# Kernel tuning notes

Measured on AMD Instinct MI355X. Metric: run time of the kernel, lower is better.

The kernel has to match this reference:

```python
import jax, jax.numpy as jnp
import numpy as np

FEATS = 32
N = FEATS + 1                      # graph nodes (node 0 = hub, 1..FEATS = leaves)
HID = FEATS * FEATS                # GRU hidden size
IN_GRU = (FEATS + 1) * FEATS * (2 * FEATS + 1)  # 33*32*65 = 68640
NEG_SLOPE = 0.2                    # DGL GATConv default leaky_relu slope


def _gat(x, W, al, ar, b):
    """DGL GATConv on the star graph (edges u->0 for all u incl. self-loop,
    plus self-loops on every node). x: [N,1]; W: [1, H*out]; al/ar: [H,out]; b: [H*out].
    Nodes 1..N-1 only receive their self-loop (softmax over one edge -> alpha=1),
    node 0 aggregates over all N source nodes."""
    H, out = al.shape
    z = (x @ W).reshape(-1, H, out)                       # [N,H,out]
    el = jnp.einsum('nho,ho->nh', z, al)                  # [N,H]
    er = jnp.einsum('nho,ho->nh', z, ar)                  # [N,H]
    e0 = jax.nn.leaky_relu(el + er[0], NEG_SLOPE)         # edges into node 0
    alpha = jax.nn.softmax(e0, axis=0)                    # softmax over N sources
    agg0 = jnp.einsum('nh,nho->ho', alpha, z)             # node-0 output
    return z.at[0].set(agg0) + b.reshape(1, H, out)


def _gru_cell(x, h, w_ih, w_hh, b_ih, b_hh):
    gi = w_ih @ x + b_ih
    gh = w_hh @ h + b_hh
    i_r, i_z, i_n = jnp.split(gi, 3)
    h_r, h_z, h_n = jnp.split(gh, 3)
    r = jax.nn.sigmoid(i_r + h_r)
    zg = jax.nn.sigmoid(i_z + h_z)
    n = jnp.tanh(i_n + r * h_n)
    return (1.0 - zg) * n + zg * h


def setup_inputs() -> dict:
    key = jax.random.key(0)
    ks = jax.random.split(key, 18)
    s = 0.05
    f32 = jnp.float32
    return {
        'data':   jax.random.normal(ks[0], (FEATS * FEATS,), f32),
        'hidden': jax.random.normal(ks[1], (2, 1, HID), f32),
        # feature GAT: in=1, out=FEATS, heads=FEATS
        'Wf':  jax.random.normal(ks[2], (1, FEATS * FEATS), f32) * s,
        'alf': jax.random.normal(ks[3], (FEATS, FEATS), f32) * s,
        'arf': jax.random.normal(ks[4], (FEATS, FEATS), f32) * s,
        'bf':  jax.random.normal(ks[5], (FEATS * FEATS,), f32) * s,
        # time GAT: in=1, out=FEATS, heads=1
        'Wt':  jax.random.normal(ks[6], (1, FEATS), f32) * s,
        'alt': jax.random.normal(ks[7], (1, FEATS), f32) * s,
        'art': jax.random.normal(ks[8], (1, FEATS), f32) * s,
        'bt':  jax.random.normal(ks[9], (FEATS,), f32) * s,
        # GRU: input IN_GRU, hidden HID, 2 layers
        'w_ih0': jax.random.normal(ks[10], (3 * HID, IN_GRU), f32) * s,
        'w_hh0': jax.random.normal(ks[11], (3 * HID, HID), f32) * s,
        'b_ih0': jax.random.normal(ks[12], (3 * HID,), f32) * s,
        'b_hh0': jax.random.normal(ks[13], (3 * HID,), f32) * s,
        'w_ih1': jax.random.normal(ks[14], (3 * HID, HID), f32) * s,
        'w_hh1': jax.random.normal(ks[15], (3 * HID, HID), f32) * s,
        'b_ih1': jax.random.normal(ks[16], (3 * HID,), f32) * s,
        'b_hh1': jax.random.normal(ks[17], (3 * HID,), f32) * s,
    }


def reference(data, hidden, Wf, alf, arf, bf, Wt, alt, art, bt,
              w_ih0, w_hh0, b_ih0, b_hh0, w_ih1, w_hh1, b_ih1, b_hh1):
    d = data.reshape(FEATS, FEATS)                         # [n_window, n_feats]
    # feature GAT on last window step, prepended with a zero for hub node 0
    data_r = jnp.concatenate([jnp.zeros((1,), d.dtype), d[-1]]).reshape(-1, 1)
    feat_r = _gat(data_r, Wf, alf, arf, bf)                # [N, FEATS, FEATS]
    # time GAT: one call per feature-row (data[:][i] == data[i]); vmapped
    Xt = jnp.concatenate([jnp.zeros((FEATS, 1), d.dtype), d], axis=1)[..., None]  # [FEATS, N, 1]
    tout = jax.vmap(lambda x: _gat(x, Wt, alt, art, bt))(Xt)  # [FEATS, N, 1, FEATS]
    time_r = tout[:, :, 0, :].transpose(1, 0, 2)           # concat on head dim -> [N, FEATS, FEATS]
    d3 = jnp.concatenate([jnp.zeros((1, FEATS), d.dtype), d]).reshape(N, FEATS, 1)
    x_in = jnp.concatenate([d3, feat_r, time_r], axis=2).reshape(-1)  # [IN_GRU]
    # 2-layer GRU, seq_len=1, batch=1
    h0 = _gru_cell(x_in, hidden[0, 0], w_ih0, w_hh0, b_ih0, b_hh0)
    h1 = _gru_cell(h0, hidden[1, 0], w_ih1, w_hh1, b_ih1, b_hh1)
    return h1, jnp.stack([h0, h1]).reshape(2, 1, HID)
```

## Files before the change

kernel.cpp:

```cpp
#include <hip/hip_runtime.h>
#include <math.h>

#define FEATS 32
#define NNODE 33
#define HID   1024
#define INGRU 68640
#define ROWS3 3072
#define N4BIG 17160
#define CHUNKS 8
#define CHLEN  2145
#define CHMAIN 2048
#define CHTAIL 97

typedef float f4 __attribute__((ext_vector_type(4)));

__device__ __forceinline__ float lrelu(float x) { return x > 0.f ? x : 0.2f * x; }
__device__ __forceinline__ float sigm(float x)  { return 1.f / (1.f + expf(-x)); }
__device__ __forceinline__ float dot4(f4 a, f4 b) {
    return a.x * b.x + a.y * b.y + a.z * b.z + a.w * b.w;
}

__global__ void __launch_bounds__(256) prep_kernel(
    const float* __restrict__ data,
    const float* __restrict__ Wf, const float* __restrict__ alf,
    const float* __restrict__ bf,
    const float* __restrict__ Wt, const float* __restrict__ alt,
    const float* __restrict__ bt,
    float* __restrict__ x_in, float* __restrict__ gi0_zero)
{
    const int n = blockIdx.x;
    const int tid = threadIdx.x;

    if (n == NNODE) {
        for (int i = tid; i < ROWS3; i += 256) gi0_zero[i] = 0.f;
        return;
    }

    __shared__ float sS[32];
    __shared__ float sSt[32];

    if (n == 0) {
        if (tid < 32) {
            float Sa = 0.f;
            for (int o = 0; o < 32; ++o) Sa += Wf[tid * 32 + o] * alf[tid * 32 + o];
            float m = 0.f;
            for (int u = 1; u <= 32; ++u)
                m = fmaxf(m, lrelu(data[31 * 32 + u - 1] * Sa));
            float den = expf(-m), num = 0.f;
            for (int u = 1; u <= 32; ++u) {
                float x = data[31 * 32 + u - 1];
                float w = expf(lrelu(x * Sa) - m);
                den += w; num += w * x;
            }
            sS[tid] = num / den;
        } else if (tid < 64) {
            const int i = tid - 32;
            float ca = 0.f;
            for (int o = 0; o < 32; ++o) ca += Wt[o] * alt[o];
            float m = 0.f;
            for (int u = 1; u <= 32; ++u)
                m = fmaxf(m, lrelu(data[i * 32 + u - 1] * ca));
            float den = expf(-m), num = 0.f;
            for (int u = 1; u <= 32; ++u) {
                float y = data[i * 32 + u - 1];
                float w = expf(lrelu(y * ca) - m);
                den += w; num += w * y;
            }
            sSt[i] = num / den;
        }
        __syncthreads();
    }

    float* out = x_in + n * 2080;
    for (int q = tid; q < 2080; q += 256) {
        const int h = q / 65, c = q % 65;
        float v;
        if (c == 0) {
            v = (n == 0) ? 0.f : data[(n - 1) * 32 + h];
        } else if (c < 33) {
            const float vf = (n == 0) ? sS[h] : data[31 * 32 + (n - 1)];
            v = vf * Wf[h * 32 + (c - 1)] + bf[h * 32 + (c - 1)];
        } else {
            const float vt = (n == 0) ? sSt[h] : data[h * 32 + (n - 1)];
            v = vt * Wt[c - 33] + bt[c - 33];
        }
        out[q] = v;
    }
}

__global__ void __launch_bounds__(256) mv_big(
    const float* __restrict__ A0, const float* __restrict__ x0,
    float* __restrict__ y0,
    const float* __restrict__ A1, const float* __restrict__ x1,
    float* __restrict__ y1)
{
    const int tid = threadIdx.x;
    float acc = 0.f;
    float* dst;
    bool is_big;

    if (blockIdx.x < ROWS3 * CHUNKS) {
        is_big = true;
        const int row = blockIdx.x >> 3, c = blockIdx.x & 7;
        const f4* A = (const f4*)A0 + (size_t)row * N4BIG + c * CHLEN;
        const f4* X = (const f4*)x0 + c * CHLEN;

        f4 a[8], x[8];
#pragma unroll
        for (int i = 0; i < 8; ++i)
            a[i] = __builtin_nontemporal_load(&A[tid + i * 256]);
#pragma unroll
        for (int i = 0; i < 8; ++i)
            x[i] = X[tid + i * 256];
        float acc2 = 0.f;
#pragma unroll
        for (int i = 0; i < 8; i += 2) {
            acc  += dot4(a[i],     x[i]);
            acc2 += dot4(a[i + 1], x[i + 1]);
        }
        if (tid < CHTAIL) {
            const f4 at = __builtin_nontemporal_load(&A[CHMAIN + tid]);
            const f4 xt = X[CHMAIN + tid];
            acc2 += dot4(at, xt);
        }
        acc += acc2;
        dst = y0 + row;
    } else {
        is_big = false;
        const int r = blockIdx.x - ROWS3 * CHUNKS;
        const f4* A = (const f4*)A1 + (size_t)r * 256;
        const f4 a = __builtin_nontemporal_load(&A[tid]);
        const f4 x = ((const f4*)x1)[tid];
        acc = dot4(a, x);
        dst = y1 + r;
    }

    for (int off = 32; off; off >>= 1) acc += __shfl_down(acc, off);
    __shared__ float red[4];
    if ((tid & 63) == 0) red[tid >> 6] = acc;
    __syncthreads();
    if (tid == 0) {
        const float tot = red[0] + red[1] + red[2] + red[3];
        if (is_big) atomicAdd(dst, tot);
        else        *dst = tot;
    }
}

__global__ void __launch_bounds__(256) mv_small(
    const float* __restrict__ A0, const float* __restrict__ x0,
    float* __restrict__ y0,
    const float* __restrict__ A1, const float* __restrict__ x1,
    float* __restrict__ y1)
{
    const int tid = threadIdx.x;
    const f4* A; const f4* X; float* dst;
    if (blockIdx.x < ROWS3) {
        A = (const f4*)A0 + (size_t)blockIdx.x * 256;
        X = (const f4*)x0;
        dst = y0 + blockIdx.x;
    } else {
        const int r = blockIdx.x - ROWS3;
        A = (const f4*)A1 + (size_t)r * 256;
        X = (const f4*)x1;
        dst = y1 + r;
    }
    const f4 a = __builtin_nontemporal_load(&A[tid]);
    const f4 x = X[tid];
    float acc = dot4(a, x);

    for (int off = 32; off; off >>= 1) acc += __shfl_down(acc, off);
    __shared__ float red[4];
    if ((tid & 63) == 0) red[tid >> 6] = acc;
    __syncthreads();
    if (tid == 0) *dst = red[0] + red[1] + red[2] + red[3];
}

__global__ void __launch_bounds__(256) gru_cell(
    const float* __restrict__ gi, const float* __restrict__ gh,
    const float* __restrict__ bih, const float* __restrict__ bhh,
    const float* __restrict__ hprev,
    float* __restrict__ hout, float* __restrict__ hout2, float* __restrict__ hout3)
{
    const int j = blockIdx.x * blockDim.x + threadIdx.x;
    const float r  = sigm(gi[j] + bih[j] + gh[j] + bhh[j]);
    const float zg = sigm(gi[HID + j] + bih[HID + j] + gh[HID + j] + bhh[HID + j]);
    const float n  = tanhf(gi[2 * HID + j] + bih[2 * HID + j]
                           + r * (gh[2 * HID + j] + bhh[2 * HID + j]));
    const float h  = (1.f - zg) * n + zg * hprev[j];
    hout[j] = h;
    if (hout2) hout2[j] = h;
    if (hout3) hout3[j] = h;
}

extern "C" void kernel_launch(void* const* d_in, const int* in_sizes, int n_in,
                              void* d_out, int out_size, void* d_ws, size_t ws_size,
                              hipStream_t stream)
{
    const float* data   = (const float*)d_in[0];
    const float* hidden = (const float*)d_in[1];
    const float* Wf     = (const float*)d_in[2];
    const float* alf    = (const float*)d_in[3];
    const float* bf     = (const float*)d_in[5];
    const float* Wt     = (const float*)d_in[6];
    const float* alt    = (const float*)d_in[7];
    const float* bt     = (const float*)d_in[9];
    const float* w_ih0  = (const float*)d_in[10];
    const float* w_hh0  = (const float*)d_in[11];
    const float* b_ih0  = (const float*)d_in[12];
    const float* b_hh0  = (const float*)d_in[13];
    const float* w_ih1  = (const float*)d_in[14];
    const float* w_hh1  = (const float*)d_in[15];
    const float* b_ih1  = (const float*)d_in[16];
    const float* b_hh1  = (const float*)d_in[17];

    float* out  = (float*)d_out;
    float* ws   = (float*)d_ws;
    float* x_in = ws;
    float* gi0  = ws + INGRU;
    float* gh0  = gi0 + ROWS3;
    float* h0   = gh0 + ROWS3;
    float* gi1  = h0 + HID;
    float* gh1  = gi1 + ROWS3;

    prep_kernel<<<NNODE + 1, 256, 0, stream>>>(data, Wf, alf, bf, Wt, alt, bt,
                                               x_in, gi0);

    mv_big<<<ROWS3 * CHUNKS + ROWS3, 256, 0, stream>>>(
        w_ih0, x_in, gi0,
        w_hh0, hidden, gh0);

    gru_cell<<<4, 256, 0, stream>>>(gi0, gh0, b_ih0, b_hh0, hidden,
                                    h0, out + HID, nullptr);

    mv_small<<<2 * ROWS3, 256, 0, stream>>>(
        w_ih1, h0, gi1,
        w_hh1, hidden + HID, gh1);

    gru_cell<<<4, 256, 0, stream>>>(gi1, gh1, b_ih1, b_hh1, hidden + HID,
                                    out, out + 2 * HID, nullptr);
}
```

Before: 171.2 us.

## Hoist hidden-state matvecs earlier to overlap with preceding stages

```diff
diff --git a/kernel.cpp b/kernel.cpp
--- a/kernel.cpp
+++ b/kernel.cpp
@@ -20,17 +20,40 @@
     return a.x * b.x + a.y * b.y + a.z * b.z + a.w * b.w;
 }
 
+__device__ __forceinline__ void block_flush(float acc, float* dst, float* red,
+                                            int tid, bool use_atomic) {
+    for (int off = 32; off; off >>= 1) acc += __shfl_down(acc, off);
+    if ((tid & 63) == 0) red[tid >> 6] = acc;
+    __syncthreads();
+    if (tid == 0) {
+        const float t = red[0] + red[1] + red[2] + red[3];
+        if (use_atomic) atomicAdd(dst, t);
+        else            *dst = t;
+    }
+}
+
 __global__ void __launch_bounds__(256) prep_kernel(
     const float* __restrict__ data,
     const float* __restrict__ Wf, const float* __restrict__ alf,
     const float* __restrict__ bf,
     const float* __restrict__ Wt, const float* __restrict__ alt,
     const float* __restrict__ bt,
-    float* __restrict__ x_in, float* __restrict__ gi0_zero)
+    float* __restrict__ x_in, float* __restrict__ gi0_zero,
+    const float* __restrict__ w_hh0, const float* __restrict__ hidden0,
+    float* __restrict__ gh0)
 {
     const int n = blockIdx.x;
     const int tid = threadIdx.x;
 
+    if (n >= NNODE + 1) {
+        const int r = n - (NNODE + 1);
+        __shared__ float red[4];
+        const f4* A = (const f4*)w_hh0 + (size_t)r * 256;
+        const f4 a = __builtin_nontemporal_load(&A[tid]);
+        const f4 x = ((const f4*)hidden0)[tid];
+        block_flush(dot4(a, x), gh0 + r, red, tid, false);
+        return;
+    }
     if (n == NNODE) {
         for (int i = tid; i < ROWS3; i += 256) gi0_zero[i] = 0.f;
         return;
@@ -98,6 +121,7 @@
     float acc = 0.f;
     float* dst;
     bool is_big;
+    __shared__ float red[4];
 
     if (blockIdx.x < ROWS3 * CHUNKS) {
         is_big = true;
@@ -135,44 +159,19 @@
         dst = y1 + r;
     }
 
-    for (int off = 32; off; off >>= 1) acc += __shfl_down(acc, off);
-    __shared__ float red[4];
-    if ((tid & 63) == 0) red[tid >> 6] = acc;
-    __syncthreads();
-    if (tid == 0) {
-        const float tot = red[0] + red[1] + red[2] + red[3];
-        if (is_big) atomicAdd(dst, tot);
-        else        *dst = tot;
-    }
+    block_flush(acc, dst, red, tid, is_big);
 }
 
 __global__ void __launch_bounds__(256) mv_small(
     const float* __restrict__ A0, const float* __restrict__ x0,
-    float* __restrict__ y0,
-    const float* __restrict__ A1, const float* __restrict__ x1,
-    float* __restrict__ y1)
+    float* __restrict__ y0)
 {
     const int tid = threadIdx.x;
-    const f4* A; const f4* X; float* dst;
-    if (blockIdx.x < ROWS3) {
-        A = (const f4*)A0 + (size_t)blockIdx.x * 256;
-        X = (const f4*)x0;
-        dst = y0 + blockIdx.x;
-    } else {
-        const int r = blockIdx.x - ROWS3;
-        A = (const f4*)A1 + (size_t)r * 256;
-        X = (const f4*)x1;
-        dst = y1 + r;
-    }
+    __shared__ float red[4];
+    const f4* A = (const f4*)A0 + (size_t)blockIdx.x * 256;
     const f4 a = __builtin_nontemporal_load(&A[tid]);
-    const f4 x = X[tid];
-    float acc = dot4(a, x);
-
-    for (int off = 32; off; off >>= 1) acc += __shfl_down(acc, off);
-    __shared__ float red[4];
-    if ((tid & 63) == 0) red[tid >> 6] = acc;
-    __syncthreads();
-    if (tid == 0) *dst = red[0] + red[1] + red[2] + red[3];
+    const f4 x = ((const f4*)x0)[tid];
+    block_flush(dot4(a, x), y0 + blockIdx.x, red, tid, false);
 }
 
 __global__ void __launch_bounds__(256) gru_cell(
@@ -222,19 +221,17 @@
     float* gi1  = h0 + HID;
     float* gh1  = gi1 + ROWS3;
 
-    prep_kernel<<<NNODE + 1, 256, 0, stream>>>(data, Wf, alf, bf, Wt, alt, bt,
-                                               x_in, gi0);
+    prep_kernel<<<NNODE + 1 + ROWS3, 256, 0, stream>>>(
+        data, Wf, alf, bf, Wt, alt, bt, x_in, gi0, w_hh0, hidden, gh0);
 
     mv_big<<<ROWS3 * CHUNKS + ROWS3, 256, 0, stream>>>(
         w_ih0, x_in, gi0,
-        w_hh0, hidden, gh0);
+        w_hh1, hidden + HID, gh1);
 
     gru_cell<<<4, 256, 0, stream>>>(gi0, gh0, b_ih0, b_hh0, hidden,
                                     h0, out + HID, nullptr);
 
-    mv_small<<<2 * ROWS3, 256, 0, stream>>>(
-        w_ih1, h0, gi1,
-        w_hh1, hidden + HID, gh1);
+    mv_small<<<ROWS3, 256, 0, stream>>>(w_ih1, h0, gi1);
 
     gru_cell<<<4, 256, 0, stream>>>(gi1, gh1, b_ih1, b_hh1, hidden + HID,
                                     out, out + 2 * HID, nullptr);
```

After: 170.2 us. No clear change (-0.6%).
